# Performance work log

Hardware: AMD Instinct MI355X
Metric: run time of the kernel (lower is better)

Reference implementation:

```python
import jax, jax.numpy as jnp
import numpy as np

B, T, D, H = 512, 129, 128, 512  # batch, T, input_size, hidden_size; T-1 = 128 steps


def setup_inputs() -> dict:
    key = jax.random.key(0)
    ks = jax.random.split(key, 7)
    s = 0.05
    return {
        "input_data": jax.random.normal(ks[0], (B, T - 1, D), jnp.float32),
        "W_ih": jax.random.normal(ks[1], (4 * H, D), jnp.float32) * s,
        "W_hh": jax.random.normal(ks[2], (4 * H, H), jnp.float32) * s,
        "b_ih": jax.random.normal(ks[3], (4 * H,), jnp.float32) * s,
        "b_hh": jax.random.normal(ks[4], (4 * H,), jnp.float32) * s,
        "attn_W": jax.random.normal(ks[5], (1, 2 * H + T - 1), jnp.float32) * s,
        "attn_b": jax.random.normal(ks[6], (1,), jnp.float32) * s,
    }


def reference(input_data, W_ih, W_hh, b_ih, b_hh, attn_W, attn_b):
    # input_data: [B, T-1, D]
    Bb, Tm1, Din = input_data.shape
    Hh = W_hh.shape[1]
    # The original concatenates [h_tiled, c_tiled, input.permute(0,2,1)] then applies a
    # Linear(2H + T-1 -> 1). That is algebraically a sum of three dot products; we split
    # the weight vector to avoid materializing the huge [B, D, 2H+T-1] concat each step.
    w = attn_W[0]
    wh, wc, wx = w[:Hh], w[Hh:2 * Hh], w[2 * Hh:]
    # input contribution to attention logits is constant over the time loop: [B, D]
    proj_x = jnp.einsum('btd,t->bd', input_data, wx)

    h0 = jnp.zeros((Bb, Hh), input_data.dtype)
    c0 = jnp.zeros((Bb, Hh), input_data.dtype)
    xs = jnp.swapaxes(input_data, 0, 1)  # [T-1, B, D]

    def step(carry, x_t):
        h, c = carry  # [B, H]
        # h/c are broadcast identically over the feature axis in the original concat,
        # so their logit contribution is a per-batch scalar.
        shift = h @ wh + c @ wc + attn_b[0]          # [B]
        logits = proj_x + shift[:, None]             # [B, D]
        attn = jax.nn.softmax(logits, axis=1)        # [B, D]
        wi = attn * x_t                              # weighted input, [B, D]
        # single-step LSTM cell (PyTorch gate order: i, f, g, o)
        gates = wi @ W_ih.T + b_ih + h @ W_hh.T + b_hh  # [B, 4H]
        i, f, g, o = jnp.split(gates, 4, axis=1)
        c_new = jax.nn.sigmoid(f) * c + jax.nn.sigmoid(i) * jnp.tanh(g)
        h_new = jax.nn.sigmoid(o) * jnp.tanh(c_new)
        return (h_new, c_new), (wi, h_new)

    _, (ws, hs) = jax.lax.scan(step, (h0, c0), xs)
    input_weighted = jnp.swapaxes(ws, 0, 1)  # [B, T-1, D]
    input_encoded = jnp.swapaxes(hs, 0, 1)   # [B, T-1, H]
    return (input_weighted, input_encoded)
```

## Files before the change

### kernel.cpp

```cpp
#include <hip/hip_runtime.h>


typedef __attribute__((ext_vector_type(8))) short short8;
typedef __attribute__((ext_vector_type(4))) float floatx4;
typedef __attribute__((ext_vector_type(4))) unsigned int uintx4;

#define NB 512
#define NT 128
#define ND 128
#define NH 512

#define HH_OFF 0
#define WT_OFF 65536
#define GT_OFF 81920
#define GT_KH  16896
#define LDS_BYTES 115712

static __device__ __forceinline__ unsigned short f2bf(float f) {
  unsigned int u = __float_as_uint(f);
  u += 0x7fffu + ((u >> 16) & 1u);
  return (unsigned short)(u >> 16);
}
static __device__ __forceinline__ float sigf(float x) {
  return 1.f / (1.f + __expf(-x));
}
static __device__ __forceinline__ float tanh_fast(float x) {
  const float e = __expf(-2.f * fabsf(x));
  const float r = (1.f - e) / (1.f + e);
  return copysignf(r, x);
}

__global__ __launch_bounds__(128) void attn_kernel(
    const float* __restrict__ in, const float* __restrict__ attn_W,
    float* __restrict__ out0, float* __restrict__ attn_ws) {
  const int b = blockIdx.x;
  const int d = threadIdx.x;
  __shared__ float wx[NT];
  __shared__ float red[4];
  wx[d] = attn_W[2 * NH + d];
  __syncthreads();
  const float* ib = in + (size_t)b * (NT * ND);
  float p = 0.f;
#pragma unroll 8
  for (int t = 0; t < NT; ++t) p = fmaf(ib[t * ND + d], wx[t], p);
  float m = p;
#pragma unroll
  for (int off = 32; off >= 1; off >>= 1) m = fmaxf(m, __shfl_xor(m, off));
  const int wv = d >> 6;
  if ((d & 63) == 0) red[wv] = m;
  __syncthreads();
  const float M = fmaxf(red[0], red[1]);
  const float e = expf(p - M);
  float s = e;
#pragma unroll
  for (int off = 32; off >= 1; off >>= 1) s += __shfl_xor(s, off);
  if ((d & 63) == 0) red[2 + wv] = s;
  __syncthreads();
  const float a = e / (red[2] + red[3]);
  attn_ws[b * ND + d] = a;
#pragma unroll 4
  for (int t = 0; t < NT; ++t)
    out0[(size_t)b * (NT * ND) + t * ND + d] = a * ib[t * ND + d];
}

__global__ __launch_bounds__(512, 2) void rec_kernel(
    const float* __restrict__ in, const float* __restrict__ W_ih,
    const float* __restrict__ W_hh, const float* __restrict__ b_ih,
    const float* __restrict__ b_hh, const float* __restrict__ attn_ws,
    unsigned short* __restrict__ hbuf, unsigned int* __restrict__ flags,
    float* __restrict__ out1) {
  __shared__ __align__(16) unsigned char LDS[LDS_BYTES];
  const int tid = threadIdx.x;
  const int bid = blockIdx.x;
  const int gid = bid & 7;
  const int sid = bid >> 3;
  const int bb0 = gid * 64;
  const int n0 = sid * 16;
  const int lane = tid & 63;
  const int wid = tid >> 6;
  const int rw = wid & 1;
  const int cg = (wid >> 1) & 1;
  const int kh = wid >> 2;
  const int colB = lane & 15;
  const int kg = lane >> 4;

  short8 bh[8][2];
  short8 bwi[2][2];
#pragma unroll
  for (int j = 0; j < 2; ++j) {
    const int gate = cg * 2 + j;
    const float* wr_h = W_hh + (size_t)(gate * NH + n0 + colB) * NH;
    const float* wr_i = W_ih + (size_t)(gate * NH + n0 + colB) * ND;
#pragma unroll
    for (int ksl = 0; ksl < 8; ++ksl) {
      const int k0 = (kh * 8 + ksl) * 32 + kg * 8;
      floatx4 f0 = *(const floatx4*)(wr_h + k0);
      floatx4 f1 = *(const floatx4*)(wr_h + k0 + 4);
      short8 s;
#pragma unroll
      for (int i = 0; i < 4; ++i) {
        s[i] = (short)f2bf(f0[i]);
        s[4 + i] = (short)f2bf(f1[i]);
      }
      bh[ksl][j] = s;
    }
#pragma unroll
    for (int ksl = 0; ksl < 2; ++ksl) {
      const int k0 = (kh * 2 + ksl) * 32 + kg * 8;
      floatx4 f0 = *(const floatx4*)(wr_i + k0);
      floatx4 f1 = *(const floatx4*)(wr_i + k0 + 4);
      short8 s;
#pragma unroll
      for (int i = 0; i < 4; ++i) {
        s[i] = (short)f2bf(f0[i]);
        s[4 + i] = (short)f2bf(f1[i]);
      }
      bwi[ksl][j] = s;
    }
  }

  const int rA = tid >> 3;
  const int pA = tid & 7;
  float areg[16];
  {
    const float* ap = attn_ws + (bb0 + rA) * ND + pA * 16;
#pragma unroll
    for (int i = 0; i < 16; ++i) areg[i] = ap[i];
  }
  const int colC = tid & 15;
  const int jC = n0 + colC;
  const float bi_i = b_ih[jC] + b_hh[jC];
  const float bi_f = b_ih[NH + jC] + b_hh[NH + jC];
  const float bi_g = b_ih[2 * NH + jC] + b_hh[2 * NH + jC];
  const float bi_o = b_ih[3 * NH + jC] + b_hh[3 * NH + jC];
  float creg0 = 0.f, creg1 = 0.f;

  const int rowa0 = rw * 32 + colB;
  const int rowa1 = rowa0 + 16;
  const int swa = (rowa0 & 7) << 4;
  unsigned int* fslot = flags + (gid * 32 + sid) * 16;
  const unsigned int* fpoll = flags + (gid * 32 + (lane & 31)) * 16;
  const int prow = tid >> 4;

  floatx4 xr4[4];
  {
    const float* xs = in + ((size_t)(bb0 + rA) * NT + 0) * ND + pA * 16;
    floatx4 xv[4];
#pragma unroll
    for (int i = 0; i < 4; ++i) xv[i] = *(const floatx4*)(xs + 4 * i);
    unsigned int w[8];
#pragma unroll
    for (int i = 0; i < 8; ++i) {
      const float v0 = xv[i >> 1][(i & 1) * 2 + 0] * areg[2 * i];
      const float v1 = xv[i >> 1][(i & 1) * 2 + 1] * areg[2 * i + 1];
      w[i] = (unsigned int)f2bf(v0) | ((unsigned int)f2bf(v1) << 16);
    }
    const int base = WT_OFF + rA * 256;
    const int swp = (rA & 7) << 4;
    uintx4 lo = {w[0], w[1], w[2], w[3]};
    uintx4 hi = {w[4], w[5], w[6], w[7]};
    *(uintx4*)&LDS[base + ((pA * 32) ^ swp)] = lo;
    *(uintx4*)&LDS[base + ((pA * 32 + 16) ^ swp)] = hi;
  }
  {
    const float* xs = in + ((size_t)(bb0 + rA) * NT + 1) * ND + pA * 16;
#pragma unroll
    for (int i = 0; i < 4; ++i) xr4[i] = *(const floatx4*)(xs + 4 * i);
  }
  __syncthreads();

  for (int t = 0; t < NT; ++t) {
    unsigned int w[8];
#pragma unroll
    for (int i = 0; i < 8; ++i) {
      const float v0 = xr4[i >> 1][(i & 1) * 2 + 0] * areg[2 * i];
      const float v1 = xr4[i >> 1][(i & 1) * 2 + 1] * areg[2 * i + 1];
      w[i] = (unsigned int)f2bf(v0) | ((unsigned int)f2bf(v1) << 16);
    }

    floatx4 acc00 = {0.f, 0.f, 0.f, 0.f};
    floatx4 acc01 = {0.f, 0.f, 0.f, 0.f};
    floatx4 acc10 = {0.f, 0.f, 0.f, 0.f};
    floatx4 acc11 = {0.f, 0.f, 0.f, 0.f};

    if (t > 0) {
      if (wid == 0) {
        unsigned int v;
        do {
          asm volatile("global_load_dword %0, %1, off sc0 sc1\n\ts_waitcnt vmcnt(0)"
                       : "=v"(v) : "v"(fpoll) : "memory");
        } while (!__all((int)v >= t));
      }
      __syncthreads();
      const unsigned short* hsrc = hbuf + (size_t)(t & 1) * (NB * NH);
      uintx4 hq[8];
#pragma unroll
      for (int p = 0; p < 8; ++p) {
        const int idx = p * 512 + tid;
        const int r = idx >> 6, s = idx & 63;
        const unsigned short* src = hsrc + (size_t)(bb0 + r) * NH + s * 8;
        asm volatile("global_load_dwordx4 %0, %1, off sc0 sc1"
                     : "=v"(hq[p]) : "v"(src) : "memory");
      }
#pragma unroll
      for (int ksl = 0; ksl < 2; ++ksl) {
        const int k2 = (kh * 2 + ksl) * 64 + kg * 16;
        short8 a0 = *(const short8*)&LDS[WT_OFF + rowa0 * 256 + (k2 ^ swa)];
        short8 a1 = *(const short8*)&LDS[WT_OFF + rowa1 * 256 + (k2 ^ swa)];
        acc00 = __builtin_amdgcn_mfma_f32_16x16x32_bf16(a0, bwi[ksl][0], acc00, 0, 0, 0);
        acc01 = __builtin_amdgcn_mfma_f32_16x16x32_bf16(a0, bwi[ksl][1], acc01, 0, 0, 0);
        acc10 = __builtin_amdgcn_mfma_f32_16x16x32_bf16(a1, bwi[ksl][0], acc10, 0, 0, 0);
        acc11 = __builtin_amdgcn_mfma_f32_16x16x32_bf16(a1, bwi[ksl][1], acc11, 0, 0, 0);
      }
      asm volatile("s_waitcnt vmcnt(0)" ::: "memory");
      __builtin_amdgcn_sched_barrier(0);
#pragma unroll
      for (int p = 0; p < 8; ++p) {
        const int idx = p * 512 + tid;
        const int r = idx >> 6, s = idx & 63;
        *(uintx4*)&LDS[HH_OFF + r * 1024 + ((s * 16) ^ ((r & 7) << 4))] = hq[p];
      }
      __syncthreads();
      {
        const int base = WT_OFF + rA * 256;
        const int swp = (rA & 7) << 4;
        uintx4 lo = {w[0], w[1], w[2], w[3]};
        uintx4 hi = {w[4], w[5], w[6], w[7]};
        *(uintx4*)&LDS[base + ((pA * 32) ^ swp)] = lo;
        *(uintx4*)&LDS[base + ((pA * 32 + 16) ^ swp)] = hi;
      }
#pragma unroll
      for (int ksl = 0; ksl < 8; ++ksl) {
        const int k2 = (kh * 8 + ksl) * 64 + kg * 16;
        short8 a0 = *(const short8*)&LDS[HH_OFF + rowa0 * 1024 + (k2 ^ swa)];
        short8 a1 = *(const short8*)&LDS[HH_OFF + rowa1 * 1024 + (k2 ^ swa)];
        acc00 = __builtin_amdgcn_mfma_f32_16x16x32_bf16(a0, bh[ksl][0], acc00, 0, 0, 0);
        acc01 = __builtin_amdgcn_mfma_f32_16x16x32_bf16(a0, bh[ksl][1], acc01, 0, 0, 0);
        acc10 = __builtin_amdgcn_mfma_f32_16x16x32_bf16(a1, bh[ksl][0], acc10, 0, 0, 0);
        acc11 = __builtin_amdgcn_mfma_f32_16x16x32_bf16(a1, bh[ksl][1], acc11, 0, 0, 0);
      }
    } else {
#pragma unroll
      for (int ksl = 0; ksl < 2; ++ksl) {
        const int k2 = (kh * 2 + ksl) * 64 + kg * 16;
        short8 a0 = *(const short8*)&LDS[WT_OFF + rowa0 * 256 + (k2 ^ swa)];
        short8 a1 = *(const short8*)&LDS[WT_OFF + rowa1 * 256 + (k2 ^ swa)];
        acc00 = __builtin_amdgcn_mfma_f32_16x16x32_bf16(a0, bwi[ksl][0], acc00, 0, 0, 0);
        acc01 = __builtin_amdgcn_mfma_f32_16x16x32_bf16(a0, bwi[ksl][1], acc01, 0, 0, 0);
        acc10 = __builtin_amdgcn_mfma_f32_16x16x32_bf16(a1, bwi[ksl][0], acc10, 0, 0, 0);
        acc11 = __builtin_amdgcn_mfma_f32_16x16x32_bf16(a1, bwi[ksl][1], acc11, 0, 0, 0);
      }
      __syncthreads();
      {
        const int base = WT_OFF + rA * 256;
        const int swp = (rA & 7) << 4;
        uintx4 lo = {w[0], w[1], w[2], w[3]};
        uintx4 hi = {w[4], w[5], w[6], w[7]};
        *(uintx4*)&LDS[base + ((pA * 32) ^ swp)] = lo;
        *(uintx4*)&LDS[base + ((pA * 32 + 16) ^ swp)] = hi;
      }
    }
#pragma unroll
    for (int i = 0; i < 2; ++i)
#pragma unroll
      for (int r = 0; r < 4; ++r) {
        const int row = rw * 32 + i * 16 + kg * 4 + r;
        const int c0 = cg * 32 + colB;
        const floatx4& aL = i ? acc10 : acc00;
        const floatx4& aR = i ? acc11 : acc01;
        *(float*)&LDS[GT_OFF + kh * GT_KH + (row * 66 + c0) * 4] = aL[r];
        *(float*)&LDS[GT_OFF + kh * GT_KH + (row * 66 + c0 + 16) * 4] = aR[r];
      }
    __syncthreads();
    float hn0, hn1;
    {
      const float* g0 = (const float*)&LDS[GT_OFF + (prow * 66) * 4];
      const float* g1 = (const float*)&LDS[GT_OFF + GT_KH + (prow * 66) * 4];
      const float gi = g0[colC] + g1[colC] + bi_i;
      const float gf = g0[16 + colC] + g1[16 + colC] + bi_f;
      const float gg = g0[32 + colC] + g1[32 + colC] + bi_g;
      const float go = g0[48 + colC] + g1[48 + colC] + bi_o;
      const float cn = sigf(gf) * creg0 + sigf(gi) * tanh_fast(gg);
      hn0 = sigf(go) * tanh_fast(cn);
      creg0 = cn;
    }
    {
      const float* g0 = (const float*)&LDS[GT_OFF + ((prow + 32) * 66) * 4];
      const float* g1 = (const float*)&LDS[GT_OFF + GT_KH + ((prow + 32) * 66) * 4];
      const float gi = g0[colC] + g1[colC] + bi_i;
      const float gf = g0[16 + colC] + g1[16 + colC] + bi_f;
      const float gg = g0[32 + colC] + g1[32 + colC] + bi_g;
      const float go = g0[48 + colC] + g1[48 + colC] + bi_o;
      const float cn = sigf(gf) * creg1 + sigf(gi) * tanh_fast(gg);
      hn1 = sigf(go) * tanh_fast(cn);
      creg1 = cn;
    }
    const unsigned int m0 = (unsigned int)f2bf(hn0);
    const unsigned int m1 = (unsigned int)f2bf(hn1);
    const unsigned int o0 = (unsigned int)__shfl_xor((int)m0, 1);
    const unsigned int o1 = (unsigned int)__shfl_xor((int)m1, 1);
    if (!(tid & 1)) {
      unsigned short* hdst = hbuf + (size_t)((t + 1) & 1) * (NB * NH);
      unsigned short* p0 = hdst + (size_t)(bb0 + prow) * NH + jC;
      unsigned short* p1 = hdst + (size_t)(bb0 + 32 + prow) * NH + jC;
      const unsigned int d0 = m0 | (o0 << 16);
      const unsigned int d1 = m1 | (o1 << 16);
      asm volatile("global_store_dword %0, %1, off sc0 sc1" :: "v"(p0), "v"(d0) : "memory");
      asm volatile("global_store_dword %0, %1, off sc0 sc1" :: "v"(p1), "v"(d1) : "memory");
    }
    asm volatile("s_waitcnt vmcnt(0)" ::: "memory");
    __syncthreads();
    if (tid == 0) {
      const unsigned int tv = (unsigned int)(t + 1);
      asm volatile("global_store_dword %0, %1, off sc0 sc1" :: "v"(fslot), "v"(tv) : "memory");
    }
    __builtin_nontemporal_store(hn0, &out1[((size_t)(bb0 + prow) * NT + t) * NH + jC]);
    __builtin_nontemporal_store(hn1, &out1[((size_t)(bb0 + 32 + prow) * NT + t) * NH + jC]);
    {
      const int tx = (t + 2 < NT) ? (t + 2) : (NT - 1);
      const float* xs = in + ((size_t)(bb0 + rA) * NT + tx) * ND + pA * 16;
#pragma unroll
      for (int i = 0; i < 4; ++i) xr4[i] = *(const floatx4*)(xs + 4 * i);
    }
  }
}

extern "C" void kernel_launch(void* const* d_in, const int* in_sizes, int n_in,
                              void* d_out, int out_size, void* d_ws, size_t ws_size,
                              hipStream_t stream) {
  (void)in_sizes; (void)n_in; (void)out_size; (void)ws_size;
  const float* in     = (const float*)d_in[0];
  const float* W_ih   = (const float*)d_in[1];
  const float* W_hh   = (const float*)d_in[2];
  const float* b_ih   = (const float*)d_in[3];
  const float* b_hh   = (const float*)d_in[4];
  const float* attn_W = (const float*)d_in[5];

  float* out0 = (float*)d_out;
  float* out1 = out0 + (size_t)NB * NT * ND;

  float* attn_ws = (float*)d_ws;
  unsigned short* hbuf = (unsigned short*)((char*)d_ws + 262144);
  unsigned int* flags = (unsigned int*)((char*)d_ws + 262144 + 1048576);

  hipMemsetAsync(flags, 0, 16384, stream);
  attn_kernel<<<NB, 128, 0, stream>>>(in, attn_W, out0, attn_ws);
  rec_kernel<<<256, 512, 0, stream>>>(in, W_ih, W_hh, b_ih, b_hh, attn_ws,
                                      hbuf, flags, out1);
}
```

Baseline: 542.6 us.

## Load h and weighted input directly into MFMA A-fragments, bypassing LDS staging

The recurrent kernel's warp tiling changes so that each wave owns 16 batch rows and all four gate tiles for half of K. Each lane then loads its MFMA A-operand fragments for h and x straight from global memory into registers, and the attention weights are multiplied in-register. This removes the LDS staging of h and the weighted input, along with one __syncthreads per step, and splits the h loads into two halves so MFMAs start before all loads land. In exchange it gives up the next-step x prefetch, issues more scattered global loads per step, and doubles the per-wave B-fragment registers.

Result: slower. 952.6 us (+75.6%).

```diff
diff --git a/kernel.cpp b/kernel.cpp
--- a/kernel.cpp
+++ b/kernel.cpp
@@ -10,11 +10,8 @@
 #define ND 128
 #define NH 512
 
-#define HH_OFF 0
-#define WT_OFF 65536
-#define GT_OFF 81920
-#define GT_KH  16896
-#define LDS_BYTES 115712
+#define GT_KH 16896
+#define LDS_BYTES 98304
 
 static __device__ __forceinline__ unsigned short f2bf(float f) {
   unsigned int u = __float_as_uint(f);
@@ -78,22 +75,20 @@
   const int n0 = sid * 16;
   const int lane = tid & 63;
   const int wid = tid >> 6;
-  const int rw = wid & 1;
-  const int cg = (wid >> 1) & 1;
+  const int rt = wid & 3;
   const int kh = wid >> 2;
   const int colB = lane & 15;
   const int kg = lane >> 4;
 
-  short8 bh[8][2];
-  short8 bwi[2][2];
-#pragma unroll
-  for (int j = 0; j < 2; ++j) {
-    const int gate = cg * 2 + j;
-    const float* wr_h = W_hh + (size_t)(gate * NH + n0 + colB) * NH;
-    const float* wr_i = W_ih + (size_t)(gate * NH + n0 + colB) * ND;
+  short8 bh[8][4];
+  short8 bwi[2][4];
+#pragma unroll
+  for (int ct = 0; ct < 4; ++ct) {
+    const float* wr_h = W_hh + (size_t)(ct * NH + n0 + colB) * NH + kh * 256;
+    const float* wr_i = W_ih + (size_t)(ct * NH + n0 + colB) * ND + kh * 64;
 #pragma unroll
     for (int ksl = 0; ksl < 8; ++ksl) {
-      const int k0 = (kh * 8 + ksl) * 32 + kg * 8;
+      const int k0 = ksl * 32 + kg * 8;
       floatx4 f0 = *(const floatx4*)(wr_h + k0);
       floatx4 f1 = *(const floatx4*)(wr_h + k0 + 4);
       short8 s;
@@ -102,11 +97,11 @@
         s[i] = (short)f2bf(f0[i]);
         s[4 + i] = (short)f2bf(f1[i]);
       }
-      bh[ksl][j] = s;
+      bh[ksl][ct] = s;
     }
 #pragma unroll
     for (int ksl = 0; ksl < 2; ++ksl) {
-      const int k0 = (kh * 2 + ksl) * 32 + kg * 8;
+      const int k0 = ksl * 32 + kg * 8;
       floatx4 f0 = *(const floatx4*)(wr_i + k0);
       floatx4 f1 = *(const floatx4*)(wr_i + k0 + 4);
       short8 s;
@@ -115,74 +110,49 @@
         s[i] = (short)f2bf(f0[i]);
         s[4 + i] = (short)f2bf(f1[i]);
       }
-      bwi[ksl][j] = s;
+      bwi[ksl][ct] = s;
     }
   }
 
-  const int rA = tid >> 3;
-  const int pA = tid & 7;
-  float areg[16];
-  {
-    const float* ap = attn_ws + (bb0 + rA) * ND + pA * 16;
-#pragma unroll
-    for (int i = 0; i < 16; ++i) areg[i] = ap[i];
+  const int brow = bb0 + rt * 16 + colB;
+  const int dbase = kh * 64 + kg * 8;
+
+  unsigned int apk[2][4];
+#pragma unroll
+  for (int ksl = 0; ksl < 2; ++ksl) {
+    const float* ap = attn_ws + (size_t)brow * ND + dbase + ksl * 32;
+#pragma unroll
+    for (int p = 0; p < 4; ++p)
+      apk[ksl][p] = (unsigned int)f2bf(ap[2 * p]) |
+                    ((unsigned int)f2bf(ap[2 * p + 1]) << 16);
   }
+
   const int colC = tid & 15;
   const int jC = n0 + colC;
+  const int prow = tid >> 4;
   const float bi_i = b_ih[jC] + b_hh[jC];
   const float bi_f = b_ih[NH + jC] + b_hh[NH + jC];
   const float bi_g = b_ih[2 * NH + jC] + b_hh[2 * NH + jC];
   const float bi_o = b_ih[3 * NH + jC] + b_hh[3 * NH + jC];
   float creg0 = 0.f, creg1 = 0.f;
 
-  const int rowa0 = rw * 32 + colB;
-  const int rowa1 = rowa0 + 16;
-  const int swa = (rowa0 & 7) << 4;
   unsigned int* fslot = flags + (gid * 32 + sid) * 16;
   const unsigned int* fpoll = flags + (gid * 32 + (lane & 31)) * 16;
-  const int prow = tid >> 4;
-
-  floatx4 xr4[4];
-  {
-    const float* xs = in + ((size_t)(bb0 + rA) * NT + 0) * ND + pA * 16;
-    floatx4 xv[4];
-#pragma unroll
-    for (int i = 0; i < 4; ++i) xv[i] = *(const floatx4*)(xs + 4 * i);
-    unsigned int w[8];
-#pragma unroll
-    for (int i = 0; i < 8; ++i) {
-      const float v0 = xv[i >> 1][(i & 1) * 2 + 0] * areg[2 * i];
-      const float v1 = xv[i >> 1][(i & 1) * 2 + 1] * areg[2 * i + 1];
-      w[i] = (unsigned int)f2bf(v0) | ((unsigned int)f2bf(v1) << 16);
-    }
-    const int base = WT_OFF + rA * 256;
-    const int swp = (rA & 7) << 4;
-    uintx4 lo = {w[0], w[1], w[2], w[3]};
-    uintx4 hi = {w[4], w[5], w[6], w[7]};
-    *(uintx4*)&LDS[base + ((pA * 32) ^ swp)] = lo;
-    *(uintx4*)&LDS[base + ((pA * 32 + 16) ^ swp)] = hi;
-  }
-  {
-    const float* xs = in + ((size_t)(bb0 + rA) * NT + 1) * ND + pA * 16;
-#pragma unroll
-    for (int i = 0; i < 4; ++i) xr4[i] = *(const floatx4*)(xs + 4 * i);
-  }
-  __syncthreads();
+
+  const unsigned short* hpA = hbuf + (size_t)brow * NH + kh * 256 + kg * 8;
+  const unsigned short* hpB = hpA + (size_t)NB * NH;
+  const float* xp = in + (size_t)brow * (NT * ND) + dbase;
+  float* o1a = out1 + (size_t)(bb0 + prow) * (NT * NH) + jC;
+  float* o1b = out1 + (size_t)(bb0 + 32 + prow) * (NT * NH) + jC;
 
   for (int t = 0; t < NT; ++t) {
-    unsigned int w[8];
-#pragma unroll
-    for (int i = 0; i < 8; ++i) {
-      const float v0 = xr4[i >> 1][(i & 1) * 2 + 0] * areg[2 * i];
-      const float v1 = xr4[i >> 1][(i & 1) * 2 + 1] * areg[2 * i + 1];
-      w[i] = (unsigned int)f2bf(v0) | ((unsigned int)f2bf(v1) << 16);
-    }
-
-    floatx4 acc00 = {0.f, 0.f, 0.f, 0.f};
-    floatx4 acc01 = {0.f, 0.f, 0.f, 0.f};
-    floatx4 acc10 = {0.f, 0.f, 0.f, 0.f};
-    floatx4 acc11 = {0.f, 0.f, 0.f, 0.f};
-
+    uintx4 xq0, xq1, xq2, xq3;
+    asm volatile("global_load_dwordx4 %0, %1, off" : "=v"(xq0) : "v"(xp) : "memory");
+    asm volatile("global_load_dwordx4 %0, %1, off offset:16" : "=v"(xq1) : "v"(xp) : "memory");
+    asm volatile("global_load_dwordx4 %0, %1, off offset:128" : "=v"(xq2) : "v"(xp) : "memory");
+    asm volatile("global_load_dwordx4 %0, %1, off offset:144" : "=v"(xq3) : "v"(xp) : "memory");
+
+    uintx4 hq0, hq1, hq2, hq3, hq4, hq5, hq6, hq7;
     if (t > 0) {
       if (wid == 0) {
         unsigned int v;
@@ -192,90 +162,92 @@
         } while (!__all((int)v >= t));
       }
       __syncthreads();
-      const unsigned short* hsrc = hbuf + (size_t)(t & 1) * (NB * NH);
-      uintx4 hq[8];
-#pragma unroll
-      for (int p = 0; p < 8; ++p) {
-        const int idx = p * 512 + tid;
-        const int r = idx >> 6, s = idx & 63;
-        const unsigned short* src = hsrc + (size_t)(bb0 + r) * NH + s * 8;
-        asm volatile("global_load_dwordx4 %0, %1, off sc0 sc1"
-                     : "=v"(hq[p]) : "v"(src) : "memory");
-      }
-#pragma unroll
-      for (int ksl = 0; ksl < 2; ++ksl) {
-        const int k2 = (kh * 2 + ksl) * 64 + kg * 16;
-        short8 a0 = *(const short8*)&LDS[WT_OFF + rowa0 * 256 + (k2 ^ swa)];
-        short8 a1 = *(const short8*)&LDS[WT_OFF + rowa1 * 256 + (k2 ^ swa)];
-        acc00 = __builtin_amdgcn_mfma_f32_16x16x32_bf16(a0, bwi[ksl][0], acc00, 0, 0, 0);
-        acc01 = __builtin_amdgcn_mfma_f32_16x16x32_bf16(a0, bwi[ksl][1], acc01, 0, 0, 0);
-        acc10 = __builtin_amdgcn_mfma_f32_16x16x32_bf16(a1, bwi[ksl][0], acc10, 0, 0, 0);
-        acc11 = __builtin_amdgcn_mfma_f32_16x16x32_bf16(a1, bwi[ksl][1], acc11, 0, 0, 0);
+      const unsigned short* hp = (t & 1) ? hpB : hpA;
+      asm volatile("global_load_dwordx4 %0, %1, off sc0 sc1" : "=v"(hq0) : "v"(hp) : "memory");
+      asm volatile("global_load_dwordx4 %0, %1, off offset:64 sc0 sc1" : "=v"(hq1) : "v"(hp) : "memory");
+      asm volatile("global_load_dwordx4 %0, %1, off offset:128 sc0 sc1" : "=v"(hq2) : "v"(hp) : "memory");
+      asm volatile("global_load_dwordx4 %0, %1, off offset:192 sc0 sc1" : "=v"(hq3) : "v"(hp) : "memory");
+      asm volatile("global_load_dwordx4 %0, %1, off offset:256 sc0 sc1" : "=v"(hq4) : "v"(hp) : "memory");
+      asm volatile("global_load_dwordx4 %0, %1, off offset:320 sc0 sc1" : "=v"(hq5) : "v"(hp) : "memory");
+      asm volatile("global_load_dwordx4 %0, %1, off offset:384 sc0 sc1" : "=v"(hq6) : "v"(hp) : "memory");
+      asm volatile("global_load_dwordx4 %0, %1, off offset:448 sc0 sc1" : "=v"(hq7) : "v"(hp) : "memory");
+      asm volatile("s_waitcnt vmcnt(8)" ::: "memory");
+    } else {
+      asm volatile("s_waitcnt vmcnt(0)" ::: "memory");
+    }
+    __builtin_amdgcn_sched_barrier(0);
+
+    floatx4 acc[4];
+#pragma unroll
+    for (int ct = 0; ct < 4; ++ct) acc[ct] = {0.f, 0.f, 0.f, 0.f};
+
+#pragma unroll
+    for (int ksl = 0; ksl < 2; ++ksl) {
+      const floatx4 x0 = __builtin_bit_cast(floatx4, ksl ? xq2 : xq0);
+      const floatx4 x1 = __builtin_bit_cast(floatx4, ksl ? xq3 : xq1);
+      float xv[8];
+#pragma unroll
+      for (int i = 0; i < 4; ++i) { xv[i] = x0[i]; xv[4 + i] = x1[i]; }
+      short8 wf;
+#pragma unroll
+      for (int p = 0; p < 4; ++p) {
+        const float a0 = __uint_as_float(apk[ksl][p] << 16);
+        const float a1 = __uint_as_float(apk[ksl][p] & 0xffff0000u);
+        wf[2 * p] = (short)f2bf(a0 * xv[2 * p]);
+        wf[2 * p + 1] = (short)f2bf(a1 * xv[2 * p + 1]);
+      }
+#pragma unroll
+      for (int ct = 0; ct < 4; ++ct)
+        acc[ct] = __builtin_amdgcn_mfma_f32_16x16x32_bf16(wf, bwi[ksl][ct], acc[ct], 0, 0, 0);
+    }
+    if (t > 0) {
+      asm volatile("s_waitcnt vmcnt(4)" ::: "memory");
+      __builtin_amdgcn_sched_barrier(0);
+      {
+        short8 a;
+        a = __builtin_bit_cast(short8, hq0);
+#pragma unroll
+        for (int ct = 0; ct < 4; ++ct) acc[ct] = __builtin_amdgcn_mfma_f32_16x16x32_bf16(a, bh[0][ct], acc[ct], 0, 0, 0);
+        a = __builtin_bit_cast(short8, hq1);
+#pragma unroll
+        for (int ct = 0; ct < 4; ++ct) acc[ct] = __builtin_amdgcn_mfma_f32_16x16x32_bf16(a, bh[1][ct], acc[ct], 0, 0, 0);
+        a = __builtin_bit_cast(short8, hq2);
+#pragma unroll
+        for (int ct = 0; ct < 4; ++ct) acc[ct] = __builtin_amdgcn_mfma_f32_16x16x32_bf16(a, bh[2][ct], acc[ct], 0, 0, 0);
+        a = __builtin_bit_cast(short8, hq3);
+#pragma unroll
+        for (int ct = 0; ct < 4; ++ct) acc[ct] = __builtin_amdgcn_mfma_f32_16x16x32_bf16(a, bh[3][ct], acc[ct], 0, 0, 0);
       }
       asm volatile("s_waitcnt vmcnt(0)" ::: "memory");
       __builtin_amdgcn_sched_barrier(0);
-#pragma unroll
-      for (int p = 0; p < 8; ++p) {
-        const int idx = p * 512 + tid;
-        const int r = idx >> 6, s = idx & 63;
-        *(uintx4*)&LDS[HH_OFF + r * 1024 + ((s * 16) ^ ((r & 7) << 4))] = hq[p];
-      }
-      __syncthreads();
       {
-        const int base = WT_OFF + rA * 256;
-        const int swp = (rA & 7) << 4;
-        uintx4 lo = {w[0], w[1], w[2], w[3]};
-        uintx4 hi = {w[4], w[5], w[6], w[7]};
-        *(uintx4*)&LDS[base + ((pA * 32) ^ swp)] = lo;
-        *(uintx4*)&LDS[base + ((pA * 32 + 16) ^ swp)] = hi;
-      }
-#pragma unroll
-      for (int ksl = 0; ksl < 8; ++ksl) {
-        const int k2 = (kh * 8 + ksl) * 64 + kg * 16;
-        short8 a0 = *(const short8*)&LDS[HH_OFF + rowa0 * 1024 + (k2 ^ swa)];
-        short8 a1 = *(const short8*)&LDS[HH_OFF + rowa1 * 1024 + (k2 ^ swa)];
-        acc00 = __builtin_amdgcn_mfma_f32_16x16x32_bf16(a0, bh[ksl][0], acc00, 0, 0, 0);
-        acc01 = __builtin_amdgcn_mfma_f32_16x16x32_bf16(a0, bh[ksl][1], acc01, 0, 0, 0);
-        acc10 = __builtin_amdgcn_mfma_f32_16x16x32_bf16(a1, bh[ksl][0], acc10, 0, 0, 0);
-        acc11 = __builtin_amdgcn_mfma_f32_16x16x32_bf16(a1, bh[ksl][1], acc11, 0, 0, 0);
-      }
-    } else {
-#pragma unroll
-      for (int ksl = 0; ksl < 2; ++ksl) {
-        const int k2 = (kh * 2 + ksl) * 64 + kg * 16;
-        short8 a0 = *(const short8*)&LDS[WT_OFF + rowa0 * 256 + (k2 ^ swa)];
-        short8 a1 = *(const short8*)&LDS[WT_OFF + rowa1 * 256 + (k2 ^ swa)];
-        acc00 = __builtin_amdgcn_mfma_f32_16x16x32_bf16(a0, bwi[ksl][0], acc00, 0, 0, 0);
-        acc01 = __builtin_amdgcn_mfma_f32_16x16x32_bf16(a0, bwi[ksl][1], acc01, 0, 0, 0);
-        acc10 = __builtin_amdgcn_mfma_f32_16x16x32_bf16(a1, bwi[ksl][0], acc10, 0, 0, 0);
-        acc11 = __builtin_amdgcn_mfma_f32_16x16x32_bf16(a1, bwi[ksl][1], acc11, 0, 0, 0);
-      }
-      __syncthreads();
-      {
-        const int base = WT_OFF + rA * 256;
-        const int swp = (rA & 7) << 4;
-        uintx4 lo = {w[0], w[1], w[2], w[3]};
-        uintx4 hi = {w[4], w[5], w[6], w[7]};
-        *(uintx4*)&LDS[base + ((pA * 32) ^ swp)] = lo;
-        *(uintx4*)&LDS[base + ((pA * 32 + 16) ^ swp)] = hi;
-      }
-    }
-#pragma unroll
-    for (int i = 0; i < 2; ++i)
+        short8 a;
+        a = __builtin_bit_cast(short8, hq4);
+#pragma unroll
+        for (int ct = 0; ct < 4; ++ct) acc[ct] = __builtin_amdgcn_mfma_f32_16x16x32_bf16(a, bh[4][ct], acc[ct], 0, 0, 0);
+        a = __builtin_bit_cast(short8, hq5);
+#pragma unroll
+        for (int ct = 0; ct < 4; ++ct) acc[ct] = __builtin_amdgcn_mfma_f32_16x16x32_bf16(a, bh[5][ct], acc[ct], 0, 0, 0);
+        a = __builtin_bit_cast(short8, hq6);
+#pragma unroll
+        for (int ct = 0; ct < 4; ++ct) acc[ct] = __builtin_amdgcn_mfma_f32_16x16x32_bf16(a, bh[6][ct], acc[ct], 0, 0, 0);
+        a = __builtin_bit_cast(short8, hq7);
+#pragma unroll
+        for (int ct = 0; ct < 4; ++ct) acc[ct] = __builtin_amdgcn_mfma_f32_16x16x32_bf16(a, bh[7][ct], acc[ct], 0, 0, 0);
+      }
+    }
+#pragma unroll
+    for (int ct = 0; ct < 4; ++ct)
 #pragma unroll
       for (int r = 0; r < 4; ++r) {
-        const int row = rw * 32 + i * 16 + kg * 4 + r;
-        const int c0 = cg * 32 + colB;
-        const floatx4& aL = i ? acc10 : acc00;
-        const floatx4& aR = i ? acc11 : acc01;
-        *(float*)&LDS[GT_OFF + kh * GT_KH + (row * 66 + c0) * 4] = aL[r];
-        *(float*)&LDS[GT_OFF + kh * GT_KH + (row * 66 + c0 + 16) * 4] = aR[r];
+        const int row = rt * 16 + kg * 4 + r;
+        *(float*)&LDS[kh * GT_KH + (row * 66 + ct * 16 + colB) * 4] = acc[ct][r];
       }
     __syncthreads();
     float hn0, hn1;
     {
-      const float* g0 = (const float*)&LDS[GT_OFF + (prow * 66) * 4];
-      const float* g1 = (const float*)&LDS[GT_OFF + GT_KH + (prow * 66) * 4];
+      const float* g0 = (const float*)&LDS[(prow * 66) * 4];
+      const float* g1 = (const float*)&LDS[GT_KH + (prow * 66) * 4];
       const float gi = g0[colC] + g1[colC] + bi_i;
       const float gf = g0[16 + colC] + g1[16 + colC] + bi_f;
       const float gg = g0[32 + colC] + g1[32 + colC] + bi_g;
@@ -285,8 +257,8 @@
       creg0 = cn;
     }
     {
-      const float* g0 = (const float*)&LDS[GT_OFF + ((prow + 32) * 66) * 4];
-      const float* g1 = (const float*)&LDS[GT_OFF + GT_KH + ((prow + 32) * 66) * 4];
+      const float* g0 = (const float*)&LDS[((prow + 32) * 66) * 4];
+      const float* g1 = (const float*)&LDS[GT_KH + ((prow + 32) * 66) * 4];
       const float gi = g0[colC] + g1[colC] + bi_i;
       const float gf = g0[16 + colC] + g1[16 + colC] + bi_f;
       const float gg = g0[32 + colC] + g1[32 + colC] + bi_g;
@@ -300,28 +272,25 @@
     const unsigned int o0 = (unsigned int)__shfl_xor((int)m0, 1);
     const unsigned int o1 = (unsigned int)__shfl_xor((int)m1, 1);
     if (!(tid & 1)) {
-      unsigned short* hdst = hbuf + (size_t)((t + 1) & 1) * (NB * NH);
-      unsigned short* p0 = hdst + (size_t)(bb0 + prow) * NH + jC;
-      unsigned short* p1 = hdst + (size_t)(bb0 + 32 + prow) * NH + jC;
+      unsigned short* hdst = hbuf + (size_t)((t + 1) & 1) * (NB * NH) +
+                             (size_t)(bb0 + prow) * NH + jC;
+      unsigned short* hdst2 = hdst + (size_t)32 * NH;
       const unsigned int d0 = m0 | (o0 << 16);
       const unsigned int d1 = m1 | (o1 << 16);
-      asm volatile("global_store_dword %0, %1, off sc0 sc1" :: "v"(p0), "v"(d0) : "memory");
-      asm volatile("global_store_dword %0, %1, off sc0 sc1" :: "v"(p1), "v"(d1) : "memory");
-    }
+      asm volatile("global_store_dword %0, %1, off sc0 sc1" :: "v"(hdst), "v"(d0) : "memory");
+      asm volatile("global_store_dword %0, %1, off sc0 sc1" :: "v"(hdst2), "v"(d1) : "memory");
+    }
+    __builtin_nontemporal_store(hn0, o1a);
+    __builtin_nontemporal_store(hn1, o1b);
     asm volatile("s_waitcnt vmcnt(0)" ::: "memory");
     __syncthreads();
     if (tid == 0) {
       const unsigned int tv = (unsigned int)(t + 1);
       asm volatile("global_store_dword %0, %1, off sc0 sc1" :: "v"(fslot), "v"(tv) : "memory");
     }
-    __builtin_nontemporal_store(hn0, &out1[((size_t)(bb0 + prow) * NT + t) * NH + jC]);
-    __builtin_nontemporal_store(hn1, &out1[((size_t)(bb0 + 32 + prow) * NT + t) * NH + jC]);
-    {
-      const int tx = (t + 2 < NT) ? (t + 2) : (NT - 1);
-      const float* xs = in + ((size_t)(bb0 + rA) * NT + tx) * ND + pA * 16;
-#pragma unroll
-      for (int i = 0; i < 4; ++i) xr4[i] = *(const floatx4*)(xs + 4 * i);
-    }
+    xp += ND;
+    o1a += NH;
+    o1b += NH;
   }
 }
 
```

## Replace per-block flag polling with per-wave atomic counter and double-buffer weighted input

Applied to the files above, without the earlier changes.

Switches the inter-block step synchronisation from per-block flag slots polled by one wave plus a block barrier to a shared per-group counter, incremented atomically by every wave and polled by every wave until it reaches t*256. The weighted-input tile is double-buffered in LDS so its MFMA can be issued before the poll and the next tile written without an extra barrier, removing one __syncthreads per step. It also uses the packed bf16 conversion instruction in place of the manual rounding. The costs are more LDS use, atomic contention on one counter, and a counter target that assumes exactly 256 waves per group.

New measurement: 1.009 ms. 85.9% more time.

```diff
diff --git a/kernel.cpp b/kernel.cpp
--- a/kernel.cpp
+++ b/kernel.cpp
@@ -11,15 +11,21 @@
 #define NH 512
 
 #define HH_OFF 0
-#define WT_OFF 65536
-#define GT_OFF 81920
+#define WT0_OFF 65536
+#define WT1_OFF 81920
+#define GT_OFF 98304
 #define GT_KH  16896
-#define LDS_BYTES 115712
+#define LDS_BYTES 132096
 
 static __device__ __forceinline__ unsigned short f2bf(float f) {
   unsigned int u = __float_as_uint(f);
   u += 0x7fffu + ((u >> 16) & 1u);
   return (unsigned short)(u >> 16);
+}
+static __device__ __forceinline__ unsigned int cvtpk(float lo, float hi) {
+  unsigned int r;
+  asm("v_cvt_pk_bf16_f32 %0, %1, %2" : "=v"(r) : "v"(lo), "v"(hi));
+  return r;
 }
 static __device__ __forceinline__ float sigf(float x) {
   return 1.f / (1.f + __expf(-x));
@@ -138,24 +144,20 @@
   const int rowa0 = rw * 32 + colB;
   const int rowa1 = rowa0 + 16;
   const int swa = (rowa0 & 7) << 4;
-  unsigned int* fslot = flags + (gid * 32 + sid) * 16;
-  const unsigned int* fpoll = flags + (gid * 32 + (lane & 31)) * 16;
   const int prow = tid >> 4;
+  unsigned int* cptr = flags + gid * 32;
 
   floatx4 xr4[4];
   {
     const float* xs = in + ((size_t)(bb0 + rA) * NT + 0) * ND + pA * 16;
-    floatx4 xv[4];
-#pragma unroll
-    for (int i = 0; i < 4; ++i) xv[i] = *(const floatx4*)(xs + 4 * i);
+#pragma unroll
+    for (int i = 0; i < 4; ++i) xr4[i] = *(const floatx4*)(xs + 4 * i);
     unsigned int w[8];
 #pragma unroll
-    for (int i = 0; i < 8; ++i) {
-      const float v0 = xv[i >> 1][(i & 1) * 2 + 0] * areg[2 * i];
-      const float v1 = xv[i >> 1][(i & 1) * 2 + 1] * areg[2 * i + 1];
-      w[i] = (unsigned int)f2bf(v0) | ((unsigned int)f2bf(v1) << 16);
-    }
-    const int base = WT_OFF + rA * 256;
+    for (int i = 0; i < 8; ++i)
+      w[i] = cvtpk(xr4[i >> 1][(i & 1) * 2 + 0] * areg[2 * i],
+                   xr4[i >> 1][(i & 1) * 2 + 1] * areg[2 * i + 1]);
+    const int base = WT0_OFF + rA * 256;
     const int swp = (rA & 7) << 4;
     uintx4 lo = {w[0], w[1], w[2], w[3]};
     uintx4 hi = {w[4], w[5], w[6], w[7]};
@@ -170,29 +172,39 @@
   __syncthreads();
 
   for (int t = 0; t < NT; ++t) {
-    unsigned int w[8];
-#pragma unroll
-    for (int i = 0; i < 8; ++i) {
-      const float v0 = xr4[i >> 1][(i & 1) * 2 + 0] * areg[2 * i];
-      const float v1 = xr4[i >> 1][(i & 1) * 2 + 1] * areg[2 * i + 1];
-      w[i] = (unsigned int)f2bf(v0) | ((unsigned int)f2bf(v1) << 16);
-    }
+    const int wtR = WT0_OFF + ((t & 1) ? (WT1_OFF - WT0_OFF) : 0);
+    const int wtW = WT0_OFF + ((t & 1) ? 0 : (WT1_OFF - WT0_OFF));
 
     floatx4 acc00 = {0.f, 0.f, 0.f, 0.f};
     floatx4 acc01 = {0.f, 0.f, 0.f, 0.f};
     floatx4 acc10 = {0.f, 0.f, 0.f, 0.f};
     floatx4 acc11 = {0.f, 0.f, 0.f, 0.f};
 
+#pragma unroll
+    for (int ksl = 0; ksl < 2; ++ksl) {
+      const int k2 = (kh * 2 + ksl) * 64 + kg * 16;
+      short8 a0 = *(const short8*)&LDS[wtR + rowa0 * 256 + (k2 ^ swa)];
+      short8 a1 = *(const short8*)&LDS[wtR + rowa1 * 256 + (k2 ^ swa)];
+      acc00 = __builtin_amdgcn_mfma_f32_16x16x32_bf16(a0, bwi[ksl][0], acc00, 0, 0, 0);
+      acc01 = __builtin_amdgcn_mfma_f32_16x16x32_bf16(a0, bwi[ksl][1], acc01, 0, 0, 0);
+      acc10 = __builtin_amdgcn_mfma_f32_16x16x32_bf16(a1, bwi[ksl][0], acc10, 0, 0, 0);
+      acc11 = __builtin_amdgcn_mfma_f32_16x16x32_bf16(a1, bwi[ksl][1], acc11, 0, 0, 0);
+    }
+    unsigned int w[8];
+#pragma unroll
+    for (int i = 0; i < 8; ++i)
+      w[i] = cvtpk(xr4[i >> 1][(i & 1) * 2 + 0] * areg[2 * i],
+                   xr4[i >> 1][(i & 1) * 2 + 1] * areg[2 * i + 1]);
+
     if (t > 0) {
-      if (wid == 0) {
-        unsigned int v;
-        do {
-          asm volatile("global_load_dword %0, %1, off sc0 sc1\n\ts_waitcnt vmcnt(0)"
-                       : "=v"(v) : "v"(fpoll) : "memory");
-        } while (!__all((int)v >= t));
-      }
-      __syncthreads();
-      const unsigned short* hsrc = hbuf + (size_t)(t & 1) * (NB * NH);
+      const unsigned int target = (unsigned int)(t << 8);
+      unsigned int v;
+      do {
+        asm volatile("global_load_dword %0, %1, off sc0 sc1\n\ts_waitcnt vmcnt(0)"
+                     : "=v"(v) : "v"(cptr) : "memory");
+      } while (v < target);
+      __builtin_amdgcn_sched_barrier(0);
+      const unsigned short* hsrc = hbuf + ((t & 1) ? (size_t)(NB * NH) : 0);
       uintx4 hq[8];
 #pragma unroll
       for (int p = 0; p < 8; ++p) {
@@ -202,16 +214,6 @@
         asm volatile("global_load_dwordx4 %0, %1, off sc0 sc1"
                      : "=v"(hq[p]) : "v"(src) : "memory");
       }
-#pragma unroll
-      for (int ksl = 0; ksl < 2; ++ksl) {
-        const int k2 = (kh * 2 + ksl) * 64 + kg * 16;
-        short8 a0 = *(const short8*)&LDS[WT_OFF + rowa0 * 256 + (k2 ^ swa)];
-        short8 a1 = *(const short8*)&LDS[WT_OFF + rowa1 * 256 + (k2 ^ swa)];
-        acc00 = __builtin_amdgcn_mfma_f32_16x16x32_bf16(a0, bwi[ksl][0], acc00, 0, 0, 0);
-        acc01 = __builtin_amdgcn_mfma_f32_16x16x32_bf16(a0, bwi[ksl][1], acc01, 0, 0, 0);
-        acc10 = __builtin_amdgcn_mfma_f32_16x16x32_bf16(a1, bwi[ksl][0], acc10, 0, 0, 0);
-        acc11 = __builtin_amdgcn_mfma_f32_16x16x32_bf16(a1, bwi[ksl][1], acc11, 0, 0, 0);
-      }
       asm volatile("s_waitcnt vmcnt(0)" ::: "memory");
       __builtin_amdgcn_sched_barrier(0);
 #pragma unroll
@@ -220,15 +222,17 @@
         const int r = idx >> 6, s = idx & 63;
         *(uintx4*)&LDS[HH_OFF + r * 1024 + ((s * 16) ^ ((r & 7) << 4))] = hq[p];
       }
-      __syncthreads();
-      {
-        const int base = WT_OFF + rA * 256;
-        const int swp = (rA & 7) << 4;
-        uintx4 lo = {w[0], w[1], w[2], w[3]};
-        uintx4 hi = {w[4], w[5], w[6], w[7]};
-        *(uintx4*)&LDS[base + ((pA * 32) ^ swp)] = lo;
-        *(uintx4*)&LDS[base + ((pA * 32 + 16) ^ swp)] = hi;
-      }
+    }
+    {
+      const int base = wtW + rA * 256;
+      const int swp = (rA & 7) << 4;
+      uintx4 lo = {w[0], w[1], w[2], w[3]};
+      uintx4 hi = {w[4], w[5], w[6], w[7]};
+      *(uintx4*)&LDS[base + ((pA * 32) ^ swp)] = lo;
+      *(uintx4*)&LDS[base + ((pA * 32 + 16) ^ swp)] = hi;
+    }
+    __syncthreads();
+    if (t > 0) {
 #pragma unroll
       for (int ksl = 0; ksl < 8; ++ksl) {
         const int k2 = (kh * 8 + ksl) * 64 + kg * 16;
@@ -238,26 +242,6 @@
         acc01 = __builtin_amdgcn_mfma_f32_16x16x32_bf16(a0, bh[ksl][1], acc01, 0, 0, 0);
         acc10 = __builtin_amdgcn_mfma_f32_16x16x32_bf16(a1, bh[ksl][0], acc10, 0, 0, 0);
         acc11 = __builtin_amdgcn_mfma_f32_16x16x32_bf16(a1, bh[ksl][1], acc11, 0, 0, 0);
-      }
-    } else {
-#pragma unroll
-      for (int ksl = 0; ksl < 2; ++ksl) {
-        const int k2 = (kh * 2 + ksl) * 64 + kg * 16;
-        short8 a0 = *(const short8*)&LDS[WT_OFF + rowa0 * 256 + (k2 ^ swa)];
-        short8 a1 = *(const short8*)&LDS[WT_OFF + rowa1 * 256 + (k2 ^ swa)];
-        acc00 = __builtin_amdgcn_mfma_f32_16x16x32_bf16(a0, bwi[ksl][0], acc00, 0, 0, 0);
-        acc01 = __builtin_amdgcn_mfma_f32_16x16x32_bf16(a0, bwi[ksl][1], acc01, 0, 0, 0);
-        acc10 = __builtin_amdgcn_mfma_f32_16x16x32_bf16(a1, bwi[ksl][0], acc10, 0, 0, 0);
-        acc11 = __builtin_amdgcn_mfma_f32_16x16x32_bf16(a1, bwi[ksl][1], acc11, 0, 0, 0);
-      }
-      __syncthreads();
-      {
-        const int base = WT_OFF + rA * 256;
-        const int swp = (rA & 7) << 4;
-        uintx4 lo = {w[0], w[1], w[2], w[3]};
-        uintx4 hi = {w[4], w[5], w[6], w[7]};
-        *(uintx4*)&LDS[base + ((pA * 32) ^ swp)] = lo;
-        *(uintx4*)&LDS[base + ((pA * 32 + 16) ^ swp)] = hi;
       }
     }
 #pragma unroll
@@ -295,25 +279,20 @@
       hn1 = sigf(go) * tanh_fast(cn);
       creg1 = cn;
     }
-    const unsigned int m0 = (unsigned int)f2bf(hn0);
-    const unsigned int m1 = (unsigned int)f2bf(hn1);
-    const unsigned int o0 = (unsigned int)__shfl_xor((int)m0, 1);
-    const unsigned int o1 = (unsigned int)__shfl_xor((int)m1, 1);
+    const float o0 = __shfl_xor(hn0, 1);
+    const float o1 = __shfl_xor(hn1, 1);
     if (!(tid & 1)) {
-      unsigned short* hdst = hbuf + (size_t)((t + 1) & 1) * (NB * NH);
-      unsigned short* p0 = hdst + (size_t)(bb0 + prow) * NH + jC;
-      unsigned short* p1 = hdst + (size_t)(bb0 + 32 + prow) * NH + jC;
-      const unsigned int d0 = m0 | (o0 << 16);
-      const unsigned int d1 = m1 | (o1 << 16);
-      asm volatile("global_store_dword %0, %1, off sc0 sc1" :: "v"(p0), "v"(d0) : "memory");
-      asm volatile("global_store_dword %0, %1, off sc0 sc1" :: "v"(p1), "v"(d1) : "memory");
+      unsigned short* hdst = hbuf + (((t + 1) & 1) ? (size_t)(NB * NH) : 0) +
+                             (size_t)(bb0 + prow) * NH + jC;
+      unsigned short* hdst2 = hdst + (size_t)32 * NH;
+      const unsigned int d0 = cvtpk(hn0, o0);
+      const unsigned int d1 = cvtpk(hn1, o1);
+      asm volatile("global_store_dword %0, %1, off sc0 sc1" :: "v"(hdst), "v"(d0) : "memory");
+      asm volatile("global_store_dword %0, %1, off sc0 sc1" :: "v"(hdst2), "v"(d1) : "memory");
     }
     asm volatile("s_waitcnt vmcnt(0)" ::: "memory");
-    __syncthreads();
-    if (tid == 0) {
-      const unsigned int tv = (unsigned int)(t + 1);
-      asm volatile("global_store_dword %0, %1, off sc0 sc1" :: "v"(fslot), "v"(tv) : "memory");
-    }
+    __builtin_amdgcn_sched_barrier(0);
+    if (lane == 0) atomicAdd(cptr, 1u);
     __builtin_nontemporal_store(hn0, &out1[((size_t)(bb0 + prow) * NT + t) * NH + jC]);
     __builtin_nontemporal_store(hn1, &out1[((size_t)(bb0 + 32 + prow) * NT + t) * NH + jC]);
     {
```
